# Kernel optimization log

Hardware: AMD Instinct MI355X
Metric: run time of the kernel (lower is better)

Reference implementation:

```python
import jax, jax.numpy as jnp
import numpy as np

NUM_HEADS = 16
HEAD_DIM = 128
POLY_ORDER = 4
LRPE_BASE = 10000.0
EPS = 1e-6


def _rope(x, offset=0):
    # x: [b, n, h, d] -- Lrpe type-1 rotary position embedding per head dim
    d = x.shape[-1]
    half = d // 2
    theta = LRPE_BASE ** (-jnp.arange(half, dtype=jnp.float32) * 2.0 / d)  # [half]
    pos = jnp.arange(x.shape[1], dtype=jnp.float32) + offset               # [n]
    ang = pos[:, None] * theta[None, :]                                    # [n, half]
    cos = jnp.cos(ang)[None, :, None, :]
    sin = jnp.sin(ang)[None, :, None, :]
    x1, x2 = x[..., :half], x[..., half:]
    return jnp.concatenate([x1 * cos - x2 * sin, x1 * sin + x2 * cos], axis=-1)


def setup_inputs() -> dict:
    key = jax.random.key(0)
    ks = jax.random.split(key, 5)
    b, n, d = 2, 2048, 2048
    std = 0.02  # init_std from module
    x = jax.random.normal(ks[0], (b, n, d), dtype=jnp.float32)
    Wq = jax.random.normal(ks[1], (d, d), dtype=jnp.float32) * std
    Wk = jax.random.normal(ks[2], (d, d), dtype=jnp.float32) * std
    Wv = jax.random.normal(ks[3], (d, d), dtype=jnp.float32) * std
    Wo = jax.random.normal(ks[4], (d, d), dtype=jnp.float32) * std
    return {"x": x, "Wq": Wq, "Wk": Wk, "Wv": Wv, "Wo": Wo}


def reference(x, Wq, Wk, Wv, Wo):
    b, n, d = x.shape
    h, hd = NUM_HEADS, HEAD_DIM
    # projections (nn.Linear: x @ W.T)
    q = (x @ Wq.T).reshape(b, n, h, hd)
    k = (x @ Wk.T).reshape(b, n, h, hd)
    v = (x @ Wv.T).reshape(b, n, h, hd)
    # LRPE (rotary, type 1), offset = 0 (no cache)
    q = _rope(q)
    k = _rope(k)
    # polynomial (non-softmax) attention: scores = (q.k)^p, causal mask,
    # row-normalized (linear-attention-style denominator)
    scores = jnp.einsum("bnhd,bmhd->bhnm", q, k) ** POLY_ORDER  # p=4 even -> >=0
    causal = jnp.tril(jnp.ones((n, n), dtype=scores.dtype))
    scores = scores * causal
    denom = jnp.maximum(scores.sum(-1, keepdims=True), EPS)      # [b,h,n,1]
    out = jnp.einsum("bhnm,bmhd->bhnd", scores, v) / denom        # [b,h,n,hd]
    out = out.transpose(0, 2, 1, 3).reshape(b, n, d)              # b n (h d)
    return out @ Wo.T
```

## Files before the change

### kernel.cpp

```cpp
#include <hip/hip_runtime.h>


typedef __bf16 bf16;
typedef __bf16 bf16x8 __attribute__((ext_vector_type(8)));
typedef __bf16 bf16x4 __attribute__((ext_vector_type(4)));
typedef float f32x4 __attribute__((ext_vector_type(4)));

#define GLD(g, l)                                                   \
  __builtin_amdgcn_global_load_lds(                                 \
      (const __attribute__((address_space(1))) void*)(g),           \
      (__attribute__((address_space(3))) void*)(l), 16, 0, 0)

#define MFMA(a, b, c) __builtin_amdgcn_mfma_f32_16x16x32_bf16(a, b, c, 0, 0, 0)

__global__ __launch_bounds__(256) void k_prep(
    const float* __restrict__ x, const float* __restrict__ Wq,
    const float* __restrict__ Wk, const float* __restrict__ Wv,
    const float* __restrict__ Wo, bf16* __restrict__ xb,
    bf16* __restrict__ wqkv, bf16* __restrict__ wob,
    float* __restrict__ ct, float* __restrict__ st) {
  const int b = blockIdx.x, tid = threadIdx.x;
  if (b < 8192) {
    int i = b * 256 + tid;
    float4 v = reinterpret_cast<const float4*>(x)[i];
    bf16x4 o = {(bf16)v.x, (bf16)v.y, (bf16)v.z, (bf16)v.w};
    reinterpret_cast<bf16x4*>(xb)[i] = o;
  } else if (b < 20480) {
    int i = (b - 8192) * 256 + tid;
    const float* src = (i < 1048576) ? Wq : ((i < 2097152) ? Wk : Wv);
    float4 v = reinterpret_cast<const float4*>(src)[i & 1048575];
    bf16x4 o = {(bf16)v.x, (bf16)v.y, (bf16)v.z, (bf16)v.w};
    reinterpret_cast<bf16x4*>(wqkv)[i] = o;
  } else if (b < 24576) {
    int i = (b - 20480) * 256 + tid;
    float4 v = reinterpret_cast<const float4*>(Wo)[i];
    bf16x4 o = {(bf16)v.x, (bf16)v.y, (bf16)v.z, (bf16)v.w};
    reinterpret_cast<bf16x4*>(wob)[i] = o;
  } else {
    int i = (b - 24576) * 256 + tid;
    int pos = i >> 6, f = i & 63;
    float theta = exp2f(-(float)f * 0.20762050593046014f);
    float ang = (float)pos * theta;
    ct[i] = cosf(ang);
    st[i] = sinf(ang);
  }
}

__global__ __launch_bounds__(256, 2) void k_gemm_qkv(
    const bf16* __restrict__ Am, const bf16* __restrict__ Bm,
    bf16* __restrict__ Qp, bf16* __restrict__ Kp, bf16* __restrict__ Vt,
    const float* __restrict__ ct, const float* __restrict__ st) {
  __shared__ __align__(16) char LDS[73728];
  const int tid = threadIdx.x, w = tid >> 6, l = tid & 63;
  const int lr = l & 15, g = l >> 4;
  const int wr = w >> 1, wc = w & 1;
  const int tm = blockIdx.y * 256, tn = blockIdx.x * 128;

  const int rl = tid >> 2;
  const int scol = (((tid & 3) ^ (rl & 3) ^ ((rl >> 2) & 3)) << 3);
  const int xo = ((g ^ (lr & 3) ^ ((lr >> 2) & 3)) << 4);

#define STAGEQ(buf, kt)                                                      \
  {                                                                          \
    _Pragma("unroll") for (int i = 0; i < 4; ++i)                            \
        GLD(Am + (size_t)(tm + i * 64 + rl) * 2048 + (kt) + scol,            \
            LDS + (buf) * 24576 + i * 4096 + tid * 16);                      \
    _Pragma("unroll") for (int i = 0; i < 2; ++i)                            \
        GLD(Bm + (size_t)(tn + i * 64 + rl) * 2048 + (kt) + scol,            \
            LDS + (buf) * 24576 + 16384 + i * 4096 + tid * 16);              \
  }

  f32x4 acc[8][4] = {};

  STAGEQ(0, 0);
  STAGEQ(1, 32);
  int cur = 0, st3 = 2;
  for (int t = 0; t < 63; ++t) {
    asm volatile("s_waitcnt vmcnt(6)" ::: "memory");
    __builtin_amdgcn_s_barrier();
    asm volatile("" ::: "memory");
    if (t < 62) STAGEQ(st3, (t + 2) * 32);
    const char* pa = LDS + cur * 24576;
    const char* pb = pa + 16384;
    bf16x8 a[8], b[4];
#pragma unroll
    for (int fm = 0; fm < 8; ++fm)
      a[fm] = *reinterpret_cast<const bf16x8*>(pa + (wr * 128 + fm * 16 + lr) * 64 + xo);
#pragma unroll
    for (int nf = 0; nf < 4; ++nf)
      b[nf] = *reinterpret_cast<const bf16x8*>(pb + (wc * 64 + nf * 16 + lr) * 64 + xo);
    __builtin_amdgcn_s_setprio(1);
#pragma unroll
    for (int fm = 0; fm < 8; ++fm)
#pragma unroll
      for (int nf = 0; nf < 4; ++nf)
        acc[fm][nf] = MFMA(a[fm], b[nf], acc[fm][nf]);
    __builtin_amdgcn_s_setprio(0);
    cur = (cur == 2) ? 0 : cur + 1;
    st3 = (st3 == 2) ? 0 : st3 + 1;
  }
  {
    asm volatile("s_waitcnt vmcnt(0)" ::: "memory");
    __builtin_amdgcn_s_barrier();
    asm volatile("" ::: "memory");
    const char* pa = LDS + cur * 24576;
    const char* pb = pa + 16384;
    bf16x8 a[8], b[4];
#pragma unroll
    for (int fm = 0; fm < 8; ++fm)
      a[fm] = *reinterpret_cast<const bf16x8*>(pa + (wr * 128 + fm * 16 + lr) * 64 + xo);
#pragma unroll
    for (int nf = 0; nf < 4; ++nf)
      b[nf] = *reinterpret_cast<const bf16x8*>(pb + (wc * 64 + nf * 16 + lr) * 64 + xo);
#pragma unroll
    for (int fm = 0; fm < 8; ++fm)
#pragma unroll
      for (int nf = 0; nf < 4; ++nf)
        acc[fm][nf] = MFMA(a[fm], b[nf], acc[fm][nf]);
  }

  if (tn < 4096) {
    __syncthreads();
    bf16* E = (bf16*)LDS;
#pragma unroll
    for (int fm = 0; fm < 8; ++fm)
#pragma unroll
      for (int nf = 0; nf < 4; ++nf)
#pragma unroll
        for (int rr = 0; rr < 4; ++rr)
          E[(wr * 128 + fm * 16 + g * 4 + rr) * 136 + wc * 64 + nf * 16 + lr] =
              (bf16)acc[fm][nf][rr];
    __syncthreads();
    const int hh = (tn & 2047) >> 7;
    bf16* dst = (tn < 2048) ? Qp : Kp;
#pragma unroll
    for (int i = 0; i < 16; ++i) {
      int task = i * 256 + tid;
      int row = task >> 4, dg = (task & 15) << 2;
      int token = tm + row, nn = token & 2047, bb = token >> 11;
      f32x4 c4 = *reinterpret_cast<const f32x4*>(ct + nn * 64 + dg);
      f32x4 s4 = *reinterpret_cast<const f32x4*>(st + nn * 64 + dg);
      bf16x4 x1 = *reinterpret_cast<const bf16x4*>(E + row * 136 + dg);
      bf16x4 x2 = *reinterpret_cast<const bf16x4*>(E + row * 136 + 64 + dg);
      bf16x4 o1, o2;
#pragma unroll
      for (int j = 0; j < 4; ++j) {
        float a1 = (float)x1[j], a2 = (float)x2[j];
        o1[j] = (bf16)(a1 * c4[j] - a2 * s4[j]);
        o2[j] = (bf16)(a1 * s4[j] + a2 * c4[j]);
      }
      size_t rb = (((size_t)bb * 16 + hh) * 2048 + nn) * 128;
      *reinterpret_cast<bf16x4*>(dst + rb + dg) = o1;
      *reinterpret_cast<bf16x4*>(dst + rb + 64 + dg) = o2;
    }
  } else {
#pragma unroll
    for (int fm = 0; fm < 8; ++fm)
#pragma unroll
      for (int nf = 0; nf < 4; ++nf) {
        int row0 = tm + wr * 128 + fm * 16 + g * 4;
        int col = (tn - 4096) + wc * 64 + nf * 16 + lr;
        int bb = row0 >> 11, nn = row0 & 2047;
        int hh = col >> 7, dd = col & 127;
        bf16x4 o = {(bf16)acc[fm][nf][0], (bf16)acc[fm][nf][1],
                    (bf16)acc[fm][nf][2], (bf16)acc[fm][nf][3]};
        *reinterpret_cast<bf16x4*>(
            Vt + (((size_t)bb * 16 + hh) * 128 + dd) * 2048 + nn) = o;
      }
  }
}

__global__ __launch_bounds__(256, 2) void k_gemm_out(const bf16* __restrict__ Am,
                                                     const bf16* __restrict__ Bm,
                                                     float* __restrict__ C) {
  __shared__ __align__(16) char LDS[73728];
  const int tid = threadIdx.x, w = tid >> 6, l = tid & 63;
  const int lr = l & 15, g = l >> 4;
  const int wr = w >> 1, wc = w & 1;
  const int tm = blockIdx.y * 256, tn = blockIdx.x * 128;

  const int rl = tid >> 2;
  const int scol = (((tid & 3) ^ (rl & 3) ^ ((rl >> 2) & 3)) << 3);
  const int xo = ((g ^ (lr & 3) ^ ((lr >> 2) & 3)) << 4);

#define STAGEU(buf, kt)                                                      \
  {                                                                          \
    _Pragma("unroll") for (int i = 0; i < 4; ++i)                            \
        GLD(Am + (size_t)(tm + i * 64 + rl) * 2048 + (kt) + scol,            \
            LDS + (buf) * 24576 + i * 4096 + tid * 16);                      \
    _Pragma("unroll") for (int i = 0; i < 2; ++i)                            \
        GLD(Bm + (size_t)(tn + i * 64 + rl) * 2048 + (kt) + scol,            \
            LDS + (buf) * 24576 + 16384 + i * 4096 + tid * 16);              \
  }

  f32x4 acc[8][4] = {};

  STAGEU(0, 0);
  STAGEU(1, 32);
  int cur = 0, st3 = 2;
  for (int t = 0; t < 63; ++t) {
    asm volatile("s_waitcnt vmcnt(6)" ::: "memory");
    __builtin_amdgcn_s_barrier();
    asm volatile("" ::: "memory");
    if (t < 62) STAGEU(st3, (t + 2) * 32);
    const char* pa = LDS + cur * 24576;
    const char* pb = pa + 16384;
    bf16x8 a[8], b[4];
#pragma unroll
    for (int fm = 0; fm < 8; ++fm)
      a[fm] = *reinterpret_cast<const bf16x8*>(pa + (wr * 128 + fm * 16 + lr) * 64 + xo);
#pragma unroll
    for (int nf = 0; nf < 4; ++nf)
      b[nf] = *reinterpret_cast<const bf16x8*>(pb + (wc * 64 + nf * 16 + lr) * 64 + xo);
    __builtin_amdgcn_s_setprio(1);
#pragma unroll
    for (int fm = 0; fm < 8; ++fm)
#pragma unroll
      for (int nf = 0; nf < 4; ++nf)
        acc[fm][nf] = MFMA(a[fm], b[nf], acc[fm][nf]);
    __builtin_amdgcn_s_setprio(0);
    cur = (cur == 2) ? 0 : cur + 1;
    st3 = (st3 == 2) ? 0 : st3 + 1;
  }
  {
    asm volatile("s_waitcnt vmcnt(0)" ::: "memory");
    __builtin_amdgcn_s_barrier();
    asm volatile("" ::: "memory");
    const char* pa = LDS + cur * 24576;
    const char* pb = pa + 16384;
    bf16x8 a[8], b[4];
#pragma unroll
    for (int fm = 0; fm < 8; ++fm)
      a[fm] = *reinterpret_cast<const bf16x8*>(pa + (wr * 128 + fm * 16 + lr) * 64 + xo);
#pragma unroll
    for (int nf = 0; nf < 4; ++nf)
      b[nf] = *reinterpret_cast<const bf16x8*>(pb + (wc * 64 + nf * 16 + lr) * 64 + xo);
#pragma unroll
    for (int fm = 0; fm < 8; ++fm)
#pragma unroll
      for (int nf = 0; nf < 4; ++nf)
        acc[fm][nf] = MFMA(a[fm], b[nf], acc[fm][nf]);
  }

#pragma unroll
  for (int fm = 0; fm < 8; ++fm)
#pragma unroll
    for (int nf = 0; nf < 4; ++nf)
#pragma unroll
      for (int rr = 0; rr < 4; ++rr) {
        int row = tm + wr * 128 + fm * 16 + g * 4 + rr;
        int col = tn + wc * 64 + nf * 16 + lr;
        C[(size_t)row * 2048 + col] = acc[fm][nf][rr];
      }
}

__global__ __launch_bounds__(256) void k_attn(const bf16* __restrict__ Q,
                                              const bf16* __restrict__ K,
                                              const bf16* __restrict__ Vt,
                                              bf16* __restrict__ O) {
  __shared__ __align__(16) bf16 Ks[2][64 * 128];
  __shared__ __align__(16) bf16 Vs[2][128 * 64];
  __shared__ __align__(16) bf16 Ps[128 * 64];
  const int tid = threadIdx.x, w = tid >> 6, l = tid & 63;
  const int lr = l & 15, g = l >> 4;
  const int qb = 15 - (blockIdx.x >> 5);
  const int bh = blockIdx.x & 31;
  const size_t base = (size_t)bh * 2048 * 128;
  const int b_ = bh >> 4, h_ = bh & 15;
  const int qbase = qb * 128;
  const int nt = 2 * qb + 2;

  bf16x8 vones = {};
  if (lr == 0) {
#pragma unroll
    for (int j = 0; j < 8; ++j) vones[j] = (bf16)1.0f;
  }

  bf16x8 qf[2][4];
#pragma unroll
  for (int mi = 0; mi < 2; ++mi)
#pragma unroll
    for (int kc = 0; kc < 4; ++kc)
      qf[mi][kc] = *reinterpret_cast<const bf16x8*>(
          Q + base + (size_t)(qbase + w * 32 + mi * 16 + lr) * 128 + kc * 32 + g * 8);

  f32x4 on[2][8] = {};
  f32x4 dn4[2] = {};

#define STAGEKV(tt, buf)                                                 \
  {                                                                      \
    const bf16* kg = K + base + (size_t)(tt) * 64 * 128;                 \
    _Pragma("unroll") for (int r = 0; r < 4; ++r) {                      \
      int row = r * 16 + w * 4 + (l >> 4);                               \
      int cc = l & 15;                                                   \
      GLD(kg + (row << 7) + ((cc ^ (row & 7)) << 3),                     \
          Ks[buf] + r * 2048 + w * 512);                                 \
    }                                                                    \
    const bf16* vg = Vt + base + (tt) * 64;                              \
    _Pragma("unroll") for (int r = 0; r < 4; ++r) {                      \
      int row = r * 32 + w * 8 + (l >> 3);                               \
      int cc = l & 7;                                                    \
      GLD(vg + (size_t)row * 2048 + ((cc ^ (row & 7)) << 3),             \
          Vs[buf] + r * 2048 + w * 512);                                 \
    }                                                                    \
  }

  STAGEKV(0, 0);

  for (int t = 0; t < nt; ++t) {
    int tn1 = (t + 1 < nt) ? t + 1 : nt - 1;
    STAGEKV(tn1, (t + 1) & 1);
    asm volatile("s_waitcnt vmcnt(8)" ::: "memory");
    __builtin_amdgcn_s_barrier();

    const bf16* kcur = Ks[t & 1];
    const bf16* vcur = Vs[t & 1];

    f32x4 s[2][4] = {};
    __builtin_amdgcn_s_setprio(1);
#pragma unroll
    for (int kc = 0; kc < 4; ++kc) {
      bf16x8 kb[4];
#pragma unroll
      for (int ni = 0; ni < 4; ++ni)
        kb[ni] = *reinterpret_cast<const bf16x8*>(
            kcur + ((ni * 16 + lr) << 7) + (((kc * 4 + g) ^ (lr & 7)) << 3));
#pragma unroll
      for (int mi = 0; mi < 2; ++mi)
#pragma unroll
        for (int ni = 0; ni < 4; ++ni)
          s[mi][ni] = MFMA(qf[mi][kc], kb[ni], s[mi][ni]);
    }
    __builtin_amdgcn_s_setprio(0);

#pragma unroll
    for (int mi = 0; mi < 2; ++mi) {
      const bool msk = (t * 64 + 63 > qbase + w * 32 + mi * 16);
#pragma unroll
      for (int ni = 0; ni < 4; ++ni)
#pragma unroll
        for (int r = 0; r < 4; ++r) {
          int lrow = mi * 16 + g * 4 + r;
          float v = s[mi][ni][r];
          if (msk) {
            int qrow = qbase + w * 32 + lrow;
            int col = t * 64 + ni * 16 + lr;
            v = (col <= qrow) ? v : 0.f;
          }
          float v2 = v * v, v4 = v2 * v2;
          Ps[((w * 32 + lrow) << 6) +
             (((ni * 2 + (lr >> 3)) ^ (lrow & 7)) << 3) + (lr & 7)] = (bf16)v4;
        }
    }

    __builtin_amdgcn_s_setprio(1);
#pragma unroll
    for (int k2 = 0; k2 < 2; ++k2) {
      bf16x8 pa[2];
#pragma unroll
      for (int mi = 0; mi < 2; ++mi)
        pa[mi] = *reinterpret_cast<const bf16x8*>(
            Ps + ((w * 32 + mi * 16 + lr) << 6) + (((k2 * 4 + g) ^ (lr & 7)) << 3));
      dn4[0] = MFMA(pa[0], vones, dn4[0]);
      dn4[1] = MFMA(pa[1], vones, dn4[1]);
#pragma unroll
      for (int ni = 0; ni < 8; ++ni) {
        bf16x8 vbf = *reinterpret_cast<const bf16x8*>(
            vcur + ((ni * 16 + lr) << 6) + (((k2 * 4 + g) ^ (lr & 7)) << 3));
        on[0][ni] = MFMA(pa[0], vbf, on[0][ni]);
        on[1][ni] = MFMA(pa[1], vbf, on[1][ni]);
      }
    }
    __builtin_amdgcn_s_setprio(0);
    __builtin_amdgcn_s_barrier();
  }

  asm volatile("s_waitcnt vmcnt(0)" ::: "memory");

#pragma unroll
  for (int mi = 0; mi < 2; ++mi)
#pragma unroll
    for (int r = 0; r < 4; ++r) {
      float d = __shfl(dn4[mi][r], l & 48);
      float inv = 1.0f / fmaxf(d, 1e-6f);
      int row = qbase + w * 32 + mi * 16 + g * 4 + r;
#pragma unroll
      for (int ni = 0; ni < 8; ++ni)
        O[((size_t)b_ * 2048 + row) * 2048 + h_ * 128 + ni * 16 + lr] =
            (bf16)(on[mi][ni][r] * inv);
    }
#undef STAGEKV
}

extern "C" void kernel_launch(void* const* d_in, const int* in_sizes, int n_in,
                              void* d_out, int out_size, void* d_ws, size_t ws_size,
                              hipStream_t stream) {
  const float* x  = (const float*)d_in[0];
  const float* Wq = (const float*)d_in[1];
  const float* Wk = (const float*)d_in[2];
  const float* Wv = (const float*)d_in[3];
  const float* Wo = (const float*)d_in[4];
  float* out = (float*)d_out;

  char* p = (char*)d_ws;
  bf16* xb   = (bf16*)p; p += (size_t)8388608 * 2;
  bf16* wqkv = (bf16*)p; p += (size_t)12582912 * 2;
  bf16* wob  = (bf16*)p; p += (size_t)4194304 * 2;
  bf16* Qp   = (bf16*)p; p += (size_t)8388608 * 2;
  bf16* Kp   = (bf16*)p; p += (size_t)8388608 * 2;
  bf16* Vt   = (bf16*)p; p += (size_t)8388608 * 2;
  bf16* Ob   = (bf16*)p; p += (size_t)8388608 * 2;
  float* ct  = (float*)p; p += (size_t)131072 * 4;
  float* st  = (float*)p; p += (size_t)131072 * 4;

  k_prep<<<25088, 256, 0, stream>>>(x, Wq, Wk, Wv, Wo, xb, wqkv, wob, ct, st);

  k_gemm_qkv<<<dim3(48, 16), 256, 0, stream>>>(xb, wqkv, Qp, Kp, Vt, ct, st);

  k_attn<<<512, 256, 0, stream>>>(Qp, Kp, Vt, Ob);

  k_gemm_out<<<dim3(16, 16), 256, 0, stream>>>(Ob, wob, out);
}
```

Baseline: 247.4 us.

## Restructure QKV GEMM into 256x256 tiles with 8-wave ping-pong pipeline

Rewrites the QKV projection GEMM to use 512-thread blocks computing 256x256 tiles with K-step 64, a two-buffer LDS schedule that interleaves global-to-LDS loads with MFMA phases under barriers, and a swizzled 1D grid for cache locality. The aim is more data reuse per tile and better overlap of memory loads with matrix math, in the style of HipKittens 8-wave ping-pong. The RoPE epilogue is split into two passes to fit the larger tile through LDS. It uses 128KB of LDS and one block per CU, which lowers occupancy and adds more barriers.

```diff
diff --git a/kernel.cpp b/kernel.cpp
--- a/kernel.cpp
+++ b/kernel.cpp
@@ -46,120 +46,233 @@
   }
 }
 
-__global__ __launch_bounds__(256, 2) void k_gemm_qkv(
+__global__ __launch_bounds__(512, 1) void k_gemm_qkv(
     const bf16* __restrict__ Am, const bf16* __restrict__ Bm,
     bf16* __restrict__ Qp, bf16* __restrict__ Kp, bf16* __restrict__ Vt,
     const float* __restrict__ ct, const float* __restrict__ st) {
-  __shared__ __align__(16) char LDS[73728];
-  const int tid = threadIdx.x, w = tid >> 6, l = tid & 63;
-  const int lr = l & 15, g = l >> 4;
-  const int wr = w >> 1, wc = w & 1;
-  const int tm = blockIdx.y * 256, tn = blockIdx.x * 128;
-
-  const int rl = tid >> 2;
-  const int scol = (((tid & 3) ^ (rl & 3) ^ ((rl >> 2) & 3)) << 3);
-  const int xo = ((g ^ (lr & 3) ^ ((lr >> 2) & 3)) << 4);
-
-#define STAGEQ(buf, kt)                                                      \
+  __shared__ __align__(16) char LDS[131072];
+  const int tid = threadIdx.x, l = tid & 63, w = tid >> 6;
+  const int lr = l & 15, g = l >> 4, lr7 = lr & 7;
+  const int wm = w >> 2, wn = w & 3;
+  const int swz = (blockIdx.x & 7) * 48 + (blockIdx.x >> 3);
+  const int tm = (swz & 15) * 256;
+  const int tn = (swz >> 4) * 256;
+
+  const int srow = tid >> 3;
+  const int ssw = ((tid & 7) ^ (srow & 7)) << 3;
+
+#define STAGE_A8(bufoff, h, kt)                                              \
   {                                                                          \
-    _Pragma("unroll") for (int i = 0; i < 4; ++i)                            \
-        GLD(Am + (size_t)(tm + i * 64 + rl) * 2048 + (kt) + scol,            \
-            LDS + (buf) * 24576 + i * 4096 + tid * 16);                      \
-    _Pragma("unroll") for (int i = 0; i < 2; ++i)                            \
-        GLD(Bm + (size_t)(tn + i * 64 + rl) * 2048 + (kt) + scol,            \
-            LDS + (buf) * 24576 + 16384 + i * 4096 + tid * 16);              \
-  }
+    GLD(Am + (size_t)(tm + (h) * 128 + srow) * 2048 + (kt) + ssw,            \
+        LDS + (bufoff) + (h) * 16384 + tid * 16);                            \
+    GLD(Am + (size_t)(tm + (h) * 128 + 64 + srow) * 2048 + (kt) + ssw,       \
+        LDS + (bufoff) + (h) * 16384 + 8192 + tid * 16);                     \
+  }
+#define STAGE_B8(bufoff, h, kt)                                              \
+  {                                                                          \
+    GLD(Bm + (size_t)(tn + (h) * 128 + srow) * 2048 + (kt) + ssw,            \
+        LDS + (bufoff) + 32768 + (h) * 16384 + tid * 16);                    \
+    GLD(Bm + (size_t)(tn + (h) * 128 + 64 + srow) * 2048 + (kt) + ssw,       \
+        LDS + (bufoff) + 32768 + (h) * 16384 + 8192 + tid * 16);             \
+  }
+
+  const int x0 = ((0 + g) ^ lr7) << 4;
+  const int x1 = ((4 + g) ^ lr7) << 4;
+  const int Ab = wm * 16384 + lr * 128;
+  const int Bb = 32768 + (wn >> 1) * 16384 + ((wn & 1) * 64 + lr) * 128;
 
   f32x4 acc[8][4] = {};
 
-  STAGEQ(0, 0);
-  STAGEQ(1, 32);
-  int cur = 0, st3 = 2;
-  for (int t = 0; t < 63; ++t) {
-    asm volatile("s_waitcnt vmcnt(6)" ::: "memory");
-    __builtin_amdgcn_s_barrier();
-    asm volatile("" ::: "memory");
-    if (t < 62) STAGEQ(st3, (t + 2) * 32);
-    const char* pa = LDS + cur * 24576;
-    const char* pb = pa + 16384;
-    bf16x8 a[8], b[4];
-#pragma unroll
-    for (int fm = 0; fm < 8; ++fm)
-      a[fm] = *reinterpret_cast<const bf16x8*>(pa + (wr * 128 + fm * 16 + lr) * 64 + xo);
+  STAGE_A8(0, 0, 0); STAGE_A8(0, 1, 0);
+  STAGE_B8(0, 0, 0); STAGE_B8(0, 1, 0);
+  STAGE_A8(65536, 0, 64); STAGE_A8(65536, 1, 64);
+  asm volatile("s_waitcnt vmcnt(4)" ::: "memory");
+  __builtin_amdgcn_s_barrier();
+
+  for (int i = 0; i < 16; ++i) {
+    const int u = 2 * i;
+    const int kodd = (u + 1) * 64;
+    const int ks2 = (u + 2 < 32 ? u + 2 : 31) * 64;
+    const int ks3 = (u + 3 < 32 ? u + 3 : 31) * 64;
+    const char* B0 = LDS;
+    const char* B1 = LDS + 65536;
+    bf16x8 a[4], a2[4], bK0[4], bK1[4];
+
 #pragma unroll
     for (int nf = 0; nf < 4; ++nf)
-      b[nf] = *reinterpret_cast<const bf16x8*>(pb + (wc * 64 + nf * 16 + lr) * 64 + xo);
-    __builtin_amdgcn_s_setprio(1);
-#pragma unroll
-    for (int fm = 0; fm < 8; ++fm)
+      bK0[nf] = *reinterpret_cast<const bf16x8*>(B0 + Bb + nf * 2048 + x0);
+#pragma unroll
+    for (int fm = 0; fm < 4; ++fm)
+      a[fm] = *reinterpret_cast<const bf16x8*>(B0 + Ab + fm * 2048 + x0);
+    STAGE_B8(65536, 0, kodd);
+    __builtin_amdgcn_s_barrier();
+    __builtin_amdgcn_s_setprio(1);
+#pragma unroll
+    for (int fm = 0; fm < 4; ++fm)
 #pragma unroll
       for (int nf = 0; nf < 4; ++nf)
-        acc[fm][nf] = MFMA(a[fm], b[nf], acc[fm][nf]);
-    __builtin_amdgcn_s_setprio(0);
-    cur = (cur == 2) ? 0 : cur + 1;
-    st3 = (st3 == 2) ? 0 : st3 + 1;
-  }
-  {
-    asm volatile("s_waitcnt vmcnt(0)" ::: "memory");
-    __builtin_amdgcn_s_barrier();
-    asm volatile("" ::: "memory");
-    const char* pa = LDS + cur * 24576;
-    const char* pb = pa + 16384;
-    bf16x8 a[8], b[4];
-#pragma unroll
-    for (int fm = 0; fm < 8; ++fm)
-      a[fm] = *reinterpret_cast<const bf16x8*>(pa + (wr * 128 + fm * 16 + lr) * 64 + xo);
+        acc[fm][nf] = MFMA(a[fm], bK0[nf], acc[fm][nf]);
+    __builtin_amdgcn_s_setprio(0);
+    __builtin_amdgcn_s_barrier();
+
 #pragma unroll
     for (int nf = 0; nf < 4; ++nf)
-      b[nf] = *reinterpret_cast<const bf16x8*>(pb + (wc * 64 + nf * 16 + lr) * 64 + xo);
-#pragma unroll
-    for (int fm = 0; fm < 8; ++fm)
+      bK1[nf] = *reinterpret_cast<const bf16x8*>(B0 + Bb + nf * 2048 + x1);
+#pragma unroll
+    for (int fm = 0; fm < 4; ++fm)
+      a2[fm] = *reinterpret_cast<const bf16x8*>(B0 + Ab + fm * 2048 + x1);
+    STAGE_B8(65536, 1, kodd);
+    __builtin_amdgcn_s_barrier();
+    __builtin_amdgcn_s_setprio(1);
+#pragma unroll
+    for (int fm = 0; fm < 4; ++fm)
 #pragma unroll
       for (int nf = 0; nf < 4; ++nf)
-        acc[fm][nf] = MFMA(a[fm], b[nf], acc[fm][nf]);
-  }
+        acc[fm][nf] = MFMA(a2[fm], bK1[nf], acc[fm][nf]);
+    __builtin_amdgcn_s_setprio(0);
+    __builtin_amdgcn_s_barrier();
+
+#pragma unroll
+    for (int fm = 0; fm < 4; ++fm)
+      a[fm] = *reinterpret_cast<const bf16x8*>(B0 + Ab + (fm + 4) * 2048 + x0);
+    STAGE_B8(0, 0, ks2);
+    __builtin_amdgcn_s_barrier();
+    __builtin_amdgcn_s_setprio(1);
+#pragma unroll
+    for (int fm = 0; fm < 4; ++fm)
+#pragma unroll
+      for (int nf = 0; nf < 4; ++nf)
+        acc[fm + 4][nf] = MFMA(a[fm], bK0[nf], acc[fm + 4][nf]);
+    __builtin_amdgcn_s_setprio(0);
+    __builtin_amdgcn_s_barrier();
+
+#pragma unroll
+    for (int fm = 0; fm < 4; ++fm)
+      a2[fm] = *reinterpret_cast<const bf16x8*>(B0 + Ab + (fm + 4) * 2048 + x1);
+    STAGE_B8(0, 1, ks2);
+    __builtin_amdgcn_s_barrier();
+    __builtin_amdgcn_s_setprio(1);
+#pragma unroll
+    for (int fm = 0; fm < 4; ++fm)
+#pragma unroll
+      for (int nf = 0; nf < 4; ++nf)
+        acc[fm + 4][nf] = MFMA(a2[fm], bK1[nf], acc[fm + 4][nf]);
+    __builtin_amdgcn_s_setprio(0);
+    asm volatile("s_waitcnt vmcnt(4)" ::: "memory");
+    __builtin_amdgcn_s_barrier();
+
+    bf16x8 aA[8], aB[8], bo[2];
+#pragma unroll
+    for (int fm = 0; fm < 8; ++fm)
+      aA[fm] = *reinterpret_cast<const bf16x8*>(B1 + Ab + fm * 2048 + x0);
+    bo[0] = *reinterpret_cast<const bf16x8*>(B1 + Bb + x0);
+    bo[1] = *reinterpret_cast<const bf16x8*>(B1 + Bb + 2048 + x0);
+    STAGE_A8(0, 0, ks2);
+    __builtin_amdgcn_s_barrier();
+    __builtin_amdgcn_s_setprio(1);
+#pragma unroll
+    for (int fm = 0; fm < 8; ++fm) {
+      acc[fm][0] = MFMA(aA[fm], bo[0], acc[fm][0]);
+      acc[fm][1] = MFMA(aA[fm], bo[1], acc[fm][1]);
+    }
+    __builtin_amdgcn_s_setprio(0);
+    __builtin_amdgcn_s_barrier();
+
+#pragma unroll
+    for (int fm = 0; fm < 8; ++fm)
+      aB[fm] = *reinterpret_cast<const bf16x8*>(B1 + Ab + fm * 2048 + x1);
+    bo[0] = *reinterpret_cast<const bf16x8*>(B1 + Bb + x1);
+    bo[1] = *reinterpret_cast<const bf16x8*>(B1 + Bb + 2048 + x1);
+    STAGE_A8(0, 1, ks2);
+    __builtin_amdgcn_s_barrier();
+    __builtin_amdgcn_s_setprio(1);
+#pragma unroll
+    for (int fm = 0; fm < 8; ++fm) {
+      acc[fm][0] = MFMA(aB[fm], bo[0], acc[fm][0]);
+      acc[fm][1] = MFMA(aB[fm], bo[1], acc[fm][1]);
+    }
+    __builtin_amdgcn_s_setprio(0);
+    __builtin_amdgcn_s_barrier();
+
+    bo[0] = *reinterpret_cast<const bf16x8*>(B1 + Bb + 2 * 2048 + x0);
+    bo[1] = *reinterpret_cast<const bf16x8*>(B1 + Bb + 3 * 2048 + x0);
+    STAGE_A8(65536, 0, ks3);
+    __builtin_amdgcn_s_barrier();
+    __builtin_amdgcn_s_setprio(1);
+#pragma unroll
+    for (int fm = 0; fm < 8; ++fm) {
+      acc[fm][2] = MFMA(aA[fm], bo[0], acc[fm][2]);
+      acc[fm][3] = MFMA(aA[fm], bo[1], acc[fm][3]);
+    }
+    __builtin_amdgcn_s_setprio(0);
+    __builtin_amdgcn_s_barrier();
+
+    bo[0] = *reinterpret_cast<const bf16x8*>(B1 + Bb + 2 * 2048 + x1);
+    bo[1] = *reinterpret_cast<const bf16x8*>(B1 + Bb + 3 * 2048 + x1);
+    STAGE_A8(65536, 1, ks3);
+    __builtin_amdgcn_s_barrier();
+    __builtin_amdgcn_s_setprio(1);
+#pragma unroll
+    for (int fm = 0; fm < 8; ++fm) {
+      acc[fm][2] = MFMA(aB[fm], bo[0], acc[fm][2]);
+      acc[fm][3] = MFMA(aB[fm], bo[1], acc[fm][3]);
+    }
+    __builtin_amdgcn_s_setprio(0);
+    asm volatile("s_waitcnt vmcnt(4)" ::: "memory");
+    __builtin_amdgcn_s_barrier();
+  }
+
+  asm volatile("s_waitcnt vmcnt(0)" ::: "memory");
+  __builtin_amdgcn_s_barrier();
 
   if (tn < 4096) {
-    __syncthreads();
+    bf16* dst = (tn < 2048) ? Qp : Kp;
+    const int nb = tn & 2047;
     bf16* E = (bf16*)LDS;
-#pragma unroll
-    for (int fm = 0; fm < 8; ++fm)
-#pragma unroll
-      for (int nf = 0; nf < 4; ++nf)
-#pragma unroll
-        for (int rr = 0; rr < 4; ++rr)
-          E[(wr * 128 + fm * 16 + g * 4 + rr) * 136 + wc * 64 + nf * 16 + lr] =
-              (bf16)acc[fm][nf][rr];
-    __syncthreads();
-    const int hh = (tn & 2047) >> 7;
-    bf16* dst = (tn < 2048) ? Qp : Kp;
-#pragma unroll
-    for (int i = 0; i < 16; ++i) {
-      int task = i * 256 + tid;
-      int row = task >> 4, dg = (task & 15) << 2;
-      int token = tm + row, nn = token & 2047, bb = token >> 11;
-      f32x4 c4 = *reinterpret_cast<const f32x4*>(ct + nn * 64 + dg);
-      f32x4 s4 = *reinterpret_cast<const f32x4*>(st + nn * 64 + dg);
-      bf16x4 x1 = *reinterpret_cast<const bf16x4*>(E + row * 136 + dg);
-      bf16x4 x2 = *reinterpret_cast<const bf16x4*>(E + row * 136 + 64 + dg);
-      bf16x4 o1, o2;
-#pragma unroll
-      for (int j = 0; j < 4; ++j) {
-        float a1 = (float)x1[j], a2 = (float)x2[j];
-        o1[j] = (bf16)(a1 * c4[j] - a2 * s4[j]);
-        o2[j] = (bf16)(a1 * s4[j] + a2 * c4[j]);
+    for (int pass = 0; pass < 2; ++pass) {
+      __syncthreads();
+      if (wm == pass) {
+#pragma unroll
+        for (int fm = 0; fm < 8; ++fm)
+#pragma unroll
+          for (int nf = 0; nf < 4; ++nf)
+#pragma unroll
+            for (int rr = 0; rr < 4; ++rr)
+              E[(fm * 16 + g * 4 + rr) * 264 + wn * 64 + nf * 16 + lr] =
+                  (bf16)acc[fm][nf][rr];
       }
-      size_t rb = (((size_t)bb * 16 + hh) * 2048 + nn) * 128;
-      *reinterpret_cast<bf16x4*>(dst + rb + dg) = o1;
-      *reinterpret_cast<bf16x4*>(dst + rb + 64 + dg) = o2;
+      __syncthreads();
+#pragma unroll
+      for (int it = 0; it < 8; ++it) {
+        int task = it * 512 + tid;
+        int row = task >> 5, rem = task & 31;
+        int hd = rem >> 4, dg = (rem & 15) << 2;
+        int token = tm + pass * 128 + row;
+        int nn = token & 2047, bb = token >> 11;
+        f32x4 c4 = *reinterpret_cast<const f32x4*>(ct + nn * 64 + dg);
+        f32x4 s4 = *reinterpret_cast<const f32x4*>(st + nn * 64 + dg);
+        bf16x4 x1v = *reinterpret_cast<const bf16x4*>(E + row * 264 + hd * 128 + dg);
+        bf16x4 x2v = *reinterpret_cast<const bf16x4*>(E + row * 264 + hd * 128 + 64 + dg);
+        bf16x4 o1, o2;
+#pragma unroll
+        for (int j = 0; j < 4; ++j) {
+          float a1 = (float)x1v[j], a2v = (float)x2v[j];
+          o1[j] = (bf16)(a1 * c4[j] - a2v * s4[j]);
+          o2[j] = (bf16)(a1 * s4[j] + a2v * c4[j]);
+        }
+        int h_ = (nb >> 7) + hd;
+        size_t rb = (((size_t)bb * 16 + h_) * 2048 + nn) * 128;
+        *reinterpret_cast<bf16x4*>(dst + rb + dg) = o1;
+        *reinterpret_cast<bf16x4*>(dst + rb + 64 + dg) = o2;
+      }
     }
   } else {
 #pragma unroll
     for (int fm = 0; fm < 8; ++fm)
 #pragma unroll
       for (int nf = 0; nf < 4; ++nf) {
-        int row0 = tm + wr * 128 + fm * 16 + g * 4;
-        int col = (tn - 4096) + wc * 64 + nf * 16 + lr;
+        int row0 = tm + wm * 128 + fm * 16 + g * 4;
+        int col = (tn - 4096) + wn * 64 + nf * 16 + lr;
         int bb = row0 >> 11, nn = row0 & 2047;
         int hh = col >> 7, dd = col & 127;
         bf16x4 o = {(bf16)acc[fm][nf][0], (bf16)acc[fm][nf][1],
@@ -415,7 +528,7 @@
 
   k_prep<<<25088, 256, 0, stream>>>(x, Wq, Wk, Wv, Wo, xb, wqkv, wob, ct, st);
 
-  k_gemm_qkv<<<dim3(48, 16), 256, 0, stream>>>(xb, wqkv, Qp, Kp, Vt, ct, st);
+  k_gemm_qkv<<<384, 512, 0, stream>>>(xb, wqkv, Qp, Kp, Vt, ct, st);
 
   k_attn<<<512, 256, 0, stream>>>(Qp, Kp, Vt, Ob);
 
```

Measured after the change: 256.0 us. +3.5%, slower.

## Shrink QKV GEMM LDS to double buffer for three blocks per CU

Applied to the files above, without the earlier changes.

Replaces the triple-buffered LDS pipeline in the QKV projection GEMM with a double buffer (48KB instead of 72KB) and raises launch bounds to three blocks per CU. The epilogue now stages the rotary output through LDS in two half-tile passes so it fits the smaller buffer. The aim is higher occupancy to hide latency. In exchange, each iteration waits for its prefetch to finish (vmcnt(0) plus a barrier), the register budget per thread is tighter and may spill, and the epilogue adds extra barriers.

```diff
diff --git a/kernel.cpp b/kernel.cpp
--- a/kernel.cpp
+++ b/kernel.cpp
@@ -46,11 +46,11 @@
   }
 }
 
-__global__ __launch_bounds__(256, 2) void k_gemm_qkv(
+__global__ __launch_bounds__(256, 3) void k_gemm_qkv(
     const bf16* __restrict__ Am, const bf16* __restrict__ Bm,
     bf16* __restrict__ Qp, bf16* __restrict__ Kp, bf16* __restrict__ Vt,
     const float* __restrict__ ct, const float* __restrict__ st) {
-  __shared__ __align__(16) char LDS[73728];
+  __shared__ __align__(16) char LDS[49152];
   const int tid = threadIdx.x, w = tid >> 6, l = tid & 63;
   const int lr = l & 15, g = l >> 4;
   const int wr = w >> 1, wc = w & 1;
@@ -73,14 +73,11 @@
   f32x4 acc[8][4] = {};
 
   STAGEQ(0, 0);
-  STAGEQ(1, 32);
-  int cur = 0, st3 = 2;
-  for (int t = 0; t < 63; ++t) {
-    asm volatile("s_waitcnt vmcnt(6)" ::: "memory");
-    __builtin_amdgcn_s_barrier();
-    asm volatile("" ::: "memory");
-    if (t < 62) STAGEQ(st3, (t + 2) * 32);
-    const char* pa = LDS + cur * 24576;
+  asm volatile("s_waitcnt vmcnt(0)" ::: "memory");
+  __builtin_amdgcn_s_barrier();
+  for (int t = 0; t < 64; ++t) {
+    if (t < 63) STAGEQ((t + 1) & 1, (t + 1) * 32);
+    const char* pa = LDS + (t & 1) * 24576;
     const char* pb = pa + 16384;
     bf16x8 a[8], b[4];
 #pragma unroll
@@ -96,62 +93,49 @@
       for (int nf = 0; nf < 4; ++nf)
         acc[fm][nf] = MFMA(a[fm], b[nf], acc[fm][nf]);
     __builtin_amdgcn_s_setprio(0);
-    cur = (cur == 2) ? 0 : cur + 1;
-    st3 = (st3 == 2) ? 0 : st3 + 1;
-  }
-  {
     asm volatile("s_waitcnt vmcnt(0)" ::: "memory");
     __builtin_amdgcn_s_barrier();
     asm volatile("" ::: "memory");
-    const char* pa = LDS + cur * 24576;
-    const char* pb = pa + 16384;
-    bf16x8 a[8], b[4];
-#pragma unroll
-    for (int fm = 0; fm < 8; ++fm)
-      a[fm] = *reinterpret_cast<const bf16x8*>(pa + (wr * 128 + fm * 16 + lr) * 64 + xo);
-#pragma unroll
-    for (int nf = 0; nf < 4; ++nf)
-      b[nf] = *reinterpret_cast<const bf16x8*>(pb + (wc * 64 + nf * 16 + lr) * 64 + xo);
-#pragma unroll
-    for (int fm = 0; fm < 8; ++fm)
-#pragma unroll
-      for (int nf = 0; nf < 4; ++nf)
-        acc[fm][nf] = MFMA(a[fm], b[nf], acc[fm][nf]);
   }
 
   if (tn < 4096) {
-    __syncthreads();
     bf16* E = (bf16*)LDS;
-#pragma unroll
-    for (int fm = 0; fm < 8; ++fm)
-#pragma unroll
-      for (int nf = 0; nf < 4; ++nf)
-#pragma unroll
-        for (int rr = 0; rr < 4; ++rr)
-          E[(wr * 128 + fm * 16 + g * 4 + rr) * 136 + wc * 64 + nf * 16 + lr] =
-              (bf16)acc[fm][nf][rr];
-    __syncthreads();
     const int hh = (tn & 2047) >> 7;
     bf16* dst = (tn < 2048) ? Qp : Kp;
-#pragma unroll
-    for (int i = 0; i < 16; ++i) {
-      int task = i * 256 + tid;
-      int row = task >> 4, dg = (task & 15) << 2;
-      int token = tm + row, nn = token & 2047, bb = token >> 11;
-      f32x4 c4 = *reinterpret_cast<const f32x4*>(ct + nn * 64 + dg);
-      f32x4 s4 = *reinterpret_cast<const f32x4*>(st + nn * 64 + dg);
-      bf16x4 x1 = *reinterpret_cast<const bf16x4*>(E + row * 136 + dg);
-      bf16x4 x2 = *reinterpret_cast<const bf16x4*>(E + row * 136 + 64 + dg);
-      bf16x4 o1, o2;
-#pragma unroll
-      for (int j = 0; j < 4; ++j) {
-        float a1 = (float)x1[j], a2 = (float)x2[j];
-        o1[j] = (bf16)(a1 * c4[j] - a2 * s4[j]);
-        o2[j] = (bf16)(a1 * s4[j] + a2 * c4[j]);
+    for (int pass = 0; pass < 2; ++pass) {
+      __syncthreads();
+      if (wr == pass) {
+#pragma unroll
+        for (int fm = 0; fm < 8; ++fm)
+#pragma unroll
+          for (int nf = 0; nf < 4; ++nf)
+#pragma unroll
+            for (int rr = 0; rr < 4; ++rr)
+              E[(fm * 16 + g * 4 + rr) * 136 + wc * 64 + nf * 16 + lr] =
+                  (bf16)acc[fm][nf][rr];
       }
-      size_t rb = (((size_t)bb * 16 + hh) * 2048 + nn) * 128;
-      *reinterpret_cast<bf16x4*>(dst + rb + dg) = o1;
-      *reinterpret_cast<bf16x4*>(dst + rb + 64 + dg) = o2;
+      __syncthreads();
+#pragma unroll
+      for (int i = 0; i < 8; ++i) {
+        int task = i * 256 + tid;
+        int row = task >> 4, dg = (task & 15) << 2;
+        int token = tm + pass * 128 + row;
+        int nn = token & 2047, bb = token >> 11;
+        f32x4 c4 = *reinterpret_cast<const f32x4*>(ct + nn * 64 + dg);
+        f32x4 s4 = *reinterpret_cast<const f32x4*>(st + nn * 64 + dg);
+        bf16x4 x1 = *reinterpret_cast<const bf16x4*>(E + row * 136 + dg);
+        bf16x4 x2 = *reinterpret_cast<const bf16x4*>(E + row * 136 + 64 + dg);
+        bf16x4 o1, o2;
+#pragma unroll
+        for (int j = 0; j < 4; ++j) {
+          float a1 = (float)x1[j], a2 = (float)x2[j];
+          o1[j] = (bf16)(a1 * c4[j] - a2 * s4[j]);
+          o2[j] = (bf16)(a1 * s4[j] + a2 * c4[j]);
+        }
+        size_t rb = (((size_t)bb * 16 + hh) * 2048 + nn) * 128;
+        *reinterpret_cast<bf16x4*>(dst + rb + dg) = o1;
+        *reinterpret_cast<bf16x4*>(dst + rb + 64 + dg) = o2;
+      }
     }
   } else {
 #pragma unroll
```

Measured after the change: 426.0 us. 1.72x slower.
